# Kernel optimization log

Measured on AMD Instinct MI355X. Metric: run time of the kernel, lower is better.

The kernel has to match this reference:

```python
import jax, jax.numpy as jnp
import numpy as np

B, S, D = 64, 8192, 128  # batch, source length, hidden (enc == dec)


def setup_inputs() -> dict:
    key = jax.random.key(0)
    ks = jax.random.split(key, 7)
    s = 1.0 / np.sqrt(D)
    return {
        "input": jax.random.normal(ks[0], (B, D), jnp.float32),
        "context": jax.random.normal(ks[1], (B, S, D), jnp.float32),
        "W_enc": jax.random.uniform(ks[2], (D, D), jnp.float32, -s, s),
        "b_enc": jax.random.uniform(ks[3], (D,), jnp.float32, -s, s),
        "W_dec": jax.random.uniform(ks[4], (D, D), jnp.float32, -s, s),
        "b_dec": jax.random.uniform(ks[5], (D,), jnp.float32, -s, s),
        "W_out": jax.random.uniform(ks[6], (D, 2 * D), jnp.float32, -s, s),  # no bias
    }


def reference(input, context, W_enc, b_enc, W_dec, b_dec, W_out):
    # projected_context = tanh(lin_encoder(context))  [B, S, D]
    pc = jnp.tanh(jnp.einsum("bse,de->bsd", context, W_enc) + b_enc)
    # q = tanh(lin_decoder(input))  [B, D]
    q = jnp.tanh(input @ W_dec.T + b_dec)
    # attention scores via bmm(projected_context, q): [B, S]
    scores = jnp.einsum("bsd,bd->bs", pc, q)
    attn = jax.nn.softmax(scores, axis=1)  # softmax over source positions
    # weighted sum of (raw) context: [B, D]
    weighted_context = jnp.einsum("bs,bsd->bd", attn, context)
    # h_tilde = tanh(linear_out(concat(weighted_context, q)))  [B, D]
    h_tilde = jnp.tanh(jnp.concatenate([weighted_context, q], axis=-1) @ W_out.T)
    return h_tilde, attn
```

## Files before the change

### kernel.cpp

```cpp
#include <hip/hip_runtime.h>
#include <hip/hip_bf16.h>

#define BB 64
#define SS 8192
#define DD 128

typedef __attribute__((ext_vector_type(8))) short bf16x8;
typedef __attribute__((ext_vector_type(4))) float f32x4;

#define SWZ(c, qd) ((qd) * 16 + ((c) ^ (2 * (qd))))

__device__ __forceinline__ unsigned pk2(float x, float y) {
    __hip_bfloat162 h = __float22bfloat162_rn(make_float2(x, y));
    union { __hip_bfloat162 h2; unsigned u; } cv;
    cv.h2 = h;
    return cv.u;
}

__device__ __forceinline__ float bflo(unsigned p) { return __uint_as_float(p << 16); }
__device__ __forceinline__ float bfhi(unsigned p) { return __uint_as_float(p & 0xffff0000u); }

__device__ __forceinline__ float tanh_fast(float x) {
    float e = __expf(2.f * x);
    return 1.f - 2.f / (e + 1.f);
}

__global__ void qproj_kernel(const float* __restrict__ input,
                             const float* __restrict__ W_dec,
                             const float* __restrict__ b_dec,
                             float* __restrict__ q) {
    __shared__ float xin[DD];
    const int b = blockIdx.x, d = threadIdx.x;
    xin[d] = input[b * DD + d];
    __syncthreads();
    const float4* wrow = (const float4*)(W_dec + (size_t)d * DD);
    float acc = 0.f;
#pragma unroll
    for (int k4 = 0; k4 < DD / 4; k4++) {
        float4 w = wrow[k4];
        float4 x = ((const float4*)xin)[k4];
        acc += w.x * x.x + w.y * x.y + w.z * x.z + w.w * x.w;
    }
    q[b * DD + d] = tanh_fast(acc + b_dec[d]);
}

__global__ __launch_bounds__(256, 3) void score_fused_kernel(
    const float* __restrict__ ctx,
    const float* __restrict__ W_enc,
    const float* __restrict__ b_enc,
    const float* __restrict__ q,
    float* __restrict__ scores,
    float* __restrict__ wcp,
    float* __restrict__ Mp,
    float* __restrict__ Tp) {
    __shared__ __align__(16) short Wl[16384];
    __shared__ __align__(16) short Cl[8192];
    __shared__ float sw[64];
    __shared__ float4 red[256];

    const int t = threadIdx.x;

    const float4* W4 = (const float4*)W_enc;
    for (int c2 = t; c2 < 2048; c2 += 256) {
        int row = c2 >> 4, kc = c2 & 15;
        float4 f0 = W4[row * 32 + kc * 2];
        float4 f1 = W4[row * 32 + kc * 2 + 1];
        int nt = row >> 4, colw = row & 15, kk = kc >> 2, qd = kc & 3;
        int a8 = (nt * 4 + kk) * 128 + SWZ(colw, qd) * 2;
        uint4 u;
        u.x = pk2(f0.x, f0.y); u.y = pk2(f0.z, f0.w);
        u.z = pk2(f1.x, f1.y); u.w = pk2(f1.z, f1.w);
        *(uint4*)&Wl[a8 * 4] = u;
    }

    const int wv = t >> 6, lane = t & 63;
    const int col = lane & 15, quad = lane >> 4;
    const int b = blockIdx.x >> 4;
    const int chunk = blockIdx.x & 15;

    const int u = t & 31, rg = t >> 5;
    const int ukk = u >> 3, uqd = (u >> 1) & 3, uh = u & 1;

    float qv[8], bv[8];
#pragma unroll
    for (int nt = 0; nt < 8; nt++) {
        qv[nt] = q[b * DD + nt * 16 + col];
        bv[nt] = b_enc[nt * 16 + col];
    }

    const float4* base = (const float4*)(ctx + ((size_t)b * SS + (size_t)chunk * 512) * DD);

    float4 R[8];
    auto pack_tile = [&]() {
#pragma unroll
        for (int i = 0; i < 8; i++) {
            int row = rg + 8 * i, w = row >> 4, c = row & 15;
            int a8 = (w * 4 + ukk) * 128 + SWZ(c, uqd) * 2 + uh;
            uint2 pk;
            pk.x = pk2(R[i].x, R[i].y);
            pk.y = pk2(R[i].z, R[i].w);
            *(uint2*)&Cl[a8 * 4] = pk;
        }
    };

#pragma unroll
    for (int i = 0; i < 8; i++) R[i] = base[t + 256 * i];
    pack_tile();
    __syncthreads();

    float Mrun = -INFINITY, Trun = 0.f;
    float4 acc4 = {0.f, 0.f, 0.f, 0.f};

    for (int it = 0; it < 8; ++it) {
        if (it < 7) {
            const float4* tb = base + (size_t)(it + 1) * 2048;
#pragma unroll
            for (int i = 0; i < 8; i++) R[i] = tb[t + 256 * i];
        }

        bf16x8 a[4];
#pragma unroll
        for (int kk = 0; kk < 4; kk++) {
            int a8 = (wv * 4 + kk) * 128 + SWZ(col, quad) * 2;
            a[kk] = *(const bf16x8*)&Cl[a8 * 4];
        }
        f32x4 acc[8];
#pragma unroll
        for (int nt = 0; nt < 8; nt++) {
            f32x4 c = {0.f, 0.f, 0.f, 0.f};
#pragma unroll
            for (int kk = 0; kk < 4; kk++) {
                int a8 = (nt * 4 + kk) * 128 + SWZ(col, quad) * 2;
                bf16x8 bf = *(const bf16x8*)&Wl[a8 * 4];
                c = __builtin_amdgcn_mfma_f32_16x16x32_bf16(a[kk], bf, c, 0, 0, 0);
            }
            acc[nt] = c;
        }

#pragma unroll
        for (int r = 0; r < 4; r++) {
            float v = 0.f;
#pragma unroll
            for (int nt = 0; nt < 8; nt++)
                v += tanh_fast(acc[nt][r] + bv[nt]) * qv[nt];
            v += __shfl_xor(v, 1);
            v += __shfl_xor(v, 2);
            v += __shfl_xor(v, 4);
            v += __shfl_xor(v, 8);
            if (col == 0) {
                int lrow = wv * 16 + quad * 4 + r;
                sw[lrow] = v;
                scores[(size_t)b * SS + chunk * 512 + it * 64 + lrow] = v;
            }
        }
        __syncthreads();

        float sv = sw[lane];
        float m = sv;
#pragma unroll
        for (int off = 1; off < 64; off <<= 1) m = fmaxf(m, __shfl_xor(m, off));
        float Mnew = fmaxf(Mrun, m);
        float alpha = __expf(Mrun - Mnew);
        float wlane = __expf(sv - Mnew);
        float ts = wlane;
#pragma unroll
        for (int off = 1; off < 64; off <<= 1) ts += __shfl_xor(ts, off);
        Trun = Trun * alpha + ts;
        Mrun = Mnew;

        acc4.x *= alpha; acc4.y *= alpha; acc4.z *= alpha; acc4.w *= alpha;
#pragma unroll
        for (int i = 0; i < 8; i++) {
            int row = rg + 8 * i, w = row >> 4, c = row & 15;
            int a8 = (w * 4 + ukk) * 128 + SWZ(c, uqd) * 2 + uh;
            uint2 pk = *(const uint2*)&Cl[a8 * 4];
            float wi = __shfl(wlane, row);
            acc4.x += wi * bflo(pk.x);
            acc4.y += wi * bfhi(pk.x);
            acc4.z += wi * bflo(pk.y);
            acc4.w += wi * bfhi(pk.y);
        }
        __syncthreads();

        if (it < 7) {
            pack_tile();
            __syncthreads();
        }
    }

    red[t] = acc4;
    __syncthreads();
    if (t < 32) {
        float4 s = red[t];
#pragma unroll
        for (int k = 1; k < 8; k++) {
            float4 p = red[t + 32 * k];
            s.x += p.x; s.y += p.y; s.z += p.z; s.w += p.w;
        }
        *(float4*)&wcp[(size_t)blockIdx.x * DD + 4 * t] = s;
    }
    if (t == 0) {
        Mp[blockIdx.x] = Mrun;
        Tp[blockIdx.x] = Trun;
    }
}

__global__ void combine_kernel(const float* __restrict__ wcp,
                               const float* __restrict__ Mp,
                               const float* __restrict__ Tp,
                               float* __restrict__ wc,
                               float* __restrict__ Ms,
                               float* __restrict__ Tinv) {
    const int b = blockIdx.x, d = threadIdx.x;
    float M = -INFINITY;
#pragma unroll
    for (int j = 0; j < 16; j++) M = fmaxf(M, Mp[b * 16 + j]);
    float T = 0.f, acc = 0.f;
#pragma unroll
    for (int j = 0; j < 16; j++) {
        float e = __expf(Mp[b * 16 + j] - M);
        T += Tp[b * 16 + j] * e;
        acc += wcp[(size_t)(b * 16 + j) * DD + d] * e;
    }
    float ti = 1.f / T;
    wc[b * DD + d] = acc * ti;
    if (d == 0) { Ms[b] = M; Tinv[b] = ti; }
}

__global__ __launch_bounds__(512) void attnfin_kernel(const float* __restrict__ scores,
                                                      const float* __restrict__ Ms,
                                                      const float* __restrict__ Tinv,
                                                      float* __restrict__ attn) {
    const int b = blockIdx.x >> 2, seg = blockIdx.x & 3;
    const float M = Ms[b], ti = Tinv[b];
    const float4* s4 = (const float4*)(scores + (size_t)b * SS) + seg * 512;
    float4* a4 = (float4*)(attn + (size_t)b * SS) + seg * 512;
    float4 v = s4[threadIdx.x];
    v.x = __expf(v.x - M) * ti;
    v.y = __expf(v.y - M) * ti;
    v.z = __expf(v.z - M) * ti;
    v.w = __expf(v.w - M) * ti;
    a4[threadIdx.x] = v;
}

__global__ void out_kernel(const float* __restrict__ wc,
                           const float* __restrict__ q,
                           const float* __restrict__ W_out,
                           float* __restrict__ h) {
    __shared__ float cat[2 * DD];
    const int b = blockIdx.x, d = threadIdx.x;
    cat[d] = wc[b * DD + d];
    cat[DD + d] = q[b * DD + d];
    __syncthreads();
    const float4* wrow = (const float4*)(W_out + (size_t)d * 2 * DD);
    float acc = 0.f;
#pragma unroll
    for (int k4 = 0; k4 < 2 * DD / 4; k4++) {
        float4 w = wrow[k4];
        float4 x = ((const float4*)cat)[k4];
        acc += w.x * x.x + w.y * x.y + w.z * x.z + w.w * x.w;
    }
    h[b * DD + d] = tanh_fast(acc);
}

extern "C" void kernel_launch(void* const* d_in, const int* in_sizes, int n_in,
                              void* d_out, int out_size, void* d_ws, size_t ws_size,
                              hipStream_t stream) {
    const float* input = (const float*)d_in[0];
    const float* ctx   = (const float*)d_in[1];
    const float* W_enc = (const float*)d_in[2];
    const float* b_enc = (const float*)d_in[3];
    const float* W_dec = (const float*)d_in[4];
    const float* b_dec = (const float*)d_in[5];
    const float* W_out = (const float*)d_in[6];

    float* h    = (float*)d_out;
    float* attn = (float*)d_out + BB * DD;

    float* ws     = (float*)d_ws;
    float* q      = ws;
    float* wc     = ws + 8192;
    float* scores = ws + 16384;
    float* wcp    = ws + 16384 + 524288;
    float* Mp     = wcp + 1024 * DD;
    float* Tp     = Mp + 1024;
    float* Ms     = Tp + 1024;
    float* Tinv   = Ms + 64;

    qproj_kernel<<<BB, DD, 0, stream>>>(input, W_dec, b_dec, q);
    score_fused_kernel<<<BB * 16, 256, 0, stream>>>(ctx, W_enc, b_enc, q,
                                                    scores, wcp, Mp, Tp);
    combine_kernel<<<BB, DD, 0, stream>>>(wcp, Mp, Tp, wc, Ms, Tinv);
    attnfin_kernel<<<BB * 4, 512, 0, stream>>>(scores, Ms, Tinv, attn);
    out_kernel<<<BB, DD, 0, stream>>>(wc, q, W_out, h);
}
```

Before: 420.9 us.

## Load context directly into MFMA fragments, drop LDS staging, double chunk count

```diff
diff --git a/kernel.cpp b/kernel.cpp
--- a/kernel.cpp
+++ b/kernel.cpp
@@ -4,6 +4,9 @@
 #define BB 64
 #define SS 8192
 #define DD 128
+#define NCHUNK 32
+#define CHROWS 256
+#define NT 4
 
 typedef __attribute__((ext_vector_type(8))) short bf16x8;
 typedef __attribute__((ext_vector_type(4))) float f32x4;
@@ -54,9 +57,8 @@
     float* __restrict__ Mp,
     float* __restrict__ Tp) {
     __shared__ __align__(16) short Wl[16384];
-    __shared__ __align__(16) short Cl[8192];
     __shared__ float sw[64];
-    __shared__ float4 red[256];
+    __shared__ float red[512];
 
     const int t = threadIdx.x;
 
@@ -75,11 +77,8 @@
 
     const int wv = t >> 6, lane = t & 63;
     const int col = lane & 15, quad = lane >> 4;
-    const int b = blockIdx.x >> 4;
-    const int chunk = blockIdx.x & 15;
-
-    const int u = t & 31, rg = t >> 5;
-    const int ukk = u >> 3, uqd = (u >> 1) & 3, uh = u & 1;
+    const int b = blockIdx.x >> 5;
+    const int chunk = blockIdx.x & 31;
 
     float qv[8], bv[8];
 #pragma unroll
@@ -88,61 +87,75 @@
         bv[nt] = b_enc[nt * 16 + col];
     }
 
-    const float4* base = (const float4*)(ctx + ((size_t)b * SS + (size_t)chunk * 512) * DD);
-
-    float4 R[8];
-    auto pack_tile = [&]() {
-#pragma unroll
-        for (int i = 0; i < 8; i++) {
-            int row = rg + 8 * i, w = row >> 4, c = row & 15;
-            int a8 = (w * 4 + ukk) * 128 + SWZ(c, uqd) * 2 + uh;
-            uint2 pk;
-            pk.x = pk2(R[i].x, R[i].y);
-            pk.y = pk2(R[i].z, R[i].w);
-            *(uint2*)&Cl[a8 * 4] = pk;
+    const float4* cbase = (const float4*)ctx
+        + ((size_t)b * SS + (size_t)chunk * CHROWS + wv * 16 + col) * (DD / 4)
+        + quad * 2;
+
+    float4 S[8];
+#pragma unroll
+    for (int kk = 0; kk < 4; kk++) {
+        S[kk * 2]     = cbase[kk * 8];
+        S[kk * 2 + 1] = cbase[kk * 8 + 1];
+    }
+
+    union FU { bf16x8 v; unsigned u[4]; };
+    FU af[4];
+    auto cvt_frags = [&]() {
+#pragma unroll
+        for (int kk = 0; kk < 4; kk++) {
+            float4 f0 = S[kk * 2], f1 = S[kk * 2 + 1];
+            af[kk].u[0] = pk2(f0.x, f0.y);
+            af[kk].u[1] = pk2(f0.z, f0.w);
+            af[kk].u[2] = pk2(f1.x, f1.y);
+            af[kk].u[3] = pk2(f1.z, f1.w);
         }
     };
-
-#pragma unroll
-    for (int i = 0; i < 8; i++) R[i] = base[t + 256 * i];
-    pack_tile();
+    cvt_frags();
     __syncthreads();
 
     float Mrun = -INFINITY, Trun = 0.f;
-    float4 acc4 = {0.f, 0.f, 0.f, 0.f};
-
-    for (int it = 0; it < 8; ++it) {
-        if (it < 7) {
-            const float4* tb = base + (size_t)(it + 1) * 2048;
-#pragma unroll
-            for (int i = 0; i < 8; i++) R[i] = tb[t + 256 * i];
-        }
-
-        bf16x8 a[4];
-#pragma unroll
-        for (int kk = 0; kk < 4; kk++) {
-            int a8 = (wv * 4 + kk) * 128 + SWZ(col, quad) * 2;
-            a[kk] = *(const bf16x8*)&Cl[a8 * 4];
-        }
-        f32x4 acc[8];
-#pragma unroll
-        for (int nt = 0; nt < 8; nt++) {
-            f32x4 c = {0.f, 0.f, 0.f, 0.f};
+    float acc32[32];
+#pragma unroll
+    for (int i = 0; i < 32; i++) acc32[i] = 0.f;
+
+    for (int it = 0; it < NT; ++it) {
+        if (it < NT - 1) {
+            const float4* nb = cbase + (size_t)(it + 1) * (64 * DD / 4);
 #pragma unroll
             for (int kk = 0; kk < 4; kk++) {
-                int a8 = (nt * 4 + kk) * 128 + SWZ(col, quad) * 2;
-                bf16x8 bf = *(const bf16x8*)&Wl[a8 * 4];
-                c = __builtin_amdgcn_mfma_f32_16x16x32_bf16(a[kk], bf, c, 0, 0, 0);
-            }
-            acc[nt] = c;
-        }
-
+                S[kk * 2]     = nb[kk * 8];
+                S[kk * 2 + 1] = nb[kk * 8 + 1];
+            }
+        }
+
+        float vr[4] = {0.f, 0.f, 0.f, 0.f};
+#pragma unroll
+        for (int h = 0; h < 2; h++) {
+            f32x4 acc[4];
+#pragma unroll
+            for (int nt = 0; nt < 4; nt++) {
+                int ntg = h * 4 + nt;
+                f32x4 c = {0.f, 0.f, 0.f, 0.f};
+#pragma unroll
+                for (int kk = 0; kk < 4; kk++) {
+                    int a8 = (ntg * 4 + kk) * 128 + SWZ(col, quad) * 2;
+                    bf16x8 bf = *(const bf16x8*)&Wl[a8 * 4];
+                    c = __builtin_amdgcn_mfma_f32_16x16x32_bf16(af[kk].v, bf, c, 0, 0, 0);
+                }
+                acc[nt] = c;
+            }
+#pragma unroll
+            for (int r = 0; r < 4; r++) {
+#pragma unroll
+                for (int nt = 0; nt < 4; nt++) {
+                    int ntg = h * 4 + nt;
+                    vr[r] += tanh_fast(acc[nt][r] + bv[ntg]) * qv[ntg];
+                }
+            }
+        }
 #pragma unroll
         for (int r = 0; r < 4; r++) {
-            float v = 0.f;
-#pragma unroll
-            for (int nt = 0; nt < 8; nt++)
-                v += tanh_fast(acc[nt][r] + bv[nt]) * qv[nt];
+            float v = vr[r];
             v += __shfl_xor(v, 1);
             v += __shfl_xor(v, 2);
             v += __shfl_xor(v, 4);
@@ -150,7 +163,7 @@
             if (col == 0) {
                 int lrow = wv * 16 + quad * 4 + r;
                 sw[lrow] = v;
-                scores[(size_t)b * SS + chunk * 512 + it * 64 + lrow] = v;
+                scores[(size_t)b * SS + (size_t)chunk * CHROWS + it * 64 + lrow] = v;
             }
         }
         __syncthreads();
@@ -168,36 +181,40 @@
         Trun = Trun * alpha + ts;
         Mrun = Mnew;
 
-        acc4.x *= alpha; acc4.y *= alpha; acc4.z *= alpha; acc4.w *= alpha;
-#pragma unroll
-        for (int i = 0; i < 8; i++) {
-            int row = rg + 8 * i, w = row >> 4, c = row & 15;
-            int a8 = (w * 4 + ukk) * 128 + SWZ(c, uqd) * 2 + uh;
-            uint2 pk = *(const uint2*)&Cl[a8 * 4];
-            float wi = __shfl(wlane, row);
-            acc4.x += wi * bflo(pk.x);
-            acc4.y += wi * bfhi(pk.x);
-            acc4.z += wi * bflo(pk.y);
-            acc4.w += wi * bfhi(pk.y);
-        }
+        float wi = __shfl(wlane, wv * 16 + col);
+#pragma unroll
+        for (int kk = 0; kk < 4; kk++) {
+#pragma unroll
+            for (int w = 0; w < 4; w++) {
+                unsigned pw = af[kk].u[w];
+                acc32[kk * 8 + 2 * w]     = acc32[kk * 8 + 2 * w] * alpha + wi * bflo(pw);
+                acc32[kk * 8 + 2 * w + 1] = acc32[kk * 8 + 2 * w + 1] * alpha + wi * bfhi(pw);
+            }
+        }
+
         __syncthreads();
 
-        if (it < 7) {
-            pack_tile();
-            __syncthreads();
-        }
-    }
-
-    red[t] = acc4;
+        if (it < NT - 1) cvt_frags();
+    }
+
+#pragma unroll
+    for (int i = 0; i < 32; i++) {
+        acc32[i] += __shfl_xor(acc32[i], 1);
+        acc32[i] += __shfl_xor(acc32[i], 2);
+        acc32[i] += __shfl_xor(acc32[i], 4);
+        acc32[i] += __shfl_xor(acc32[i], 8);
+    }
+    if (col == 0) {
+#pragma unroll
+        for (int kk = 0; kk < 4; kk++)
+#pragma unroll
+            for (int j = 0; j < 8; j++)
+                red[wv * 128 + kk * 32 + quad * 8 + j] = acc32[kk * 8 + j];
+    }
     __syncthreads();
-    if (t < 32) {
-        float4 s = red[t];
-#pragma unroll
-        for (int k = 1; k < 8; k++) {
-            float4 p = red[t + 32 * k];
-            s.x += p.x; s.y += p.y; s.z += p.z; s.w += p.w;
-        }
-        *(float4*)&wcp[(size_t)blockIdx.x * DD + 4 * t] = s;
+    if (t < 128) {
+        float s = red[t] + red[128 + t] + red[256 + t] + red[384 + t];
+        wcp[(size_t)blockIdx.x * DD + t] = s;
     }
     if (t == 0) {
         Mp[blockIdx.x] = Mrun;
@@ -205,26 +222,40 @@
     }
 }
 
-__global__ void combine_kernel(const float* __restrict__ wcp,
-                               const float* __restrict__ Mp,
-                               const float* __restrict__ Tp,
-                               float* __restrict__ wc,
-                               float* __restrict__ Ms,
-                               float* __restrict__ Tinv) {
+__global__ void combine_out_kernel(const float* __restrict__ wcp,
+                                   const float* __restrict__ Mp,
+                                   const float* __restrict__ Tp,
+                                   const float* __restrict__ q,
+                                   const float* __restrict__ W_out,
+                                   float* __restrict__ h,
+                                   float* __restrict__ Ms,
+                                   float* __restrict__ Tinv) {
+    __shared__ float cat[2 * DD];
     const int b = blockIdx.x, d = threadIdx.x;
     float M = -INFINITY;
 #pragma unroll
-    for (int j = 0; j < 16; j++) M = fmaxf(M, Mp[b * 16 + j]);
+    for (int j = 0; j < NCHUNK; j++) M = fmaxf(M, Mp[b * NCHUNK + j]);
     float T = 0.f, acc = 0.f;
 #pragma unroll
-    for (int j = 0; j < 16; j++) {
-        float e = __expf(Mp[b * 16 + j] - M);
-        T += Tp[b * 16 + j] * e;
-        acc += wcp[(size_t)(b * 16 + j) * DD + d] * e;
+    for (int j = 0; j < NCHUNK; j++) {
+        float e = __expf(Mp[b * NCHUNK + j] - M);
+        T += Tp[b * NCHUNK + j] * e;
+        acc += wcp[(size_t)(b * NCHUNK + j) * DD + d] * e;
     }
     float ti = 1.f / T;
-    wc[b * DD + d] = acc * ti;
+    cat[d] = acc * ti;
+    cat[DD + d] = q[b * DD + d];
     if (d == 0) { Ms[b] = M; Tinv[b] = ti; }
+    __syncthreads();
+    const float4* wrow = (const float4*)(W_out + (size_t)d * 2 * DD);
+    float a2 = 0.f;
+#pragma unroll
+    for (int k4 = 0; k4 < 2 * DD / 4; k4++) {
+        float4 w = wrow[k4];
+        float4 x = ((const float4*)cat)[k4];
+        a2 += w.x * x.x + w.y * x.y + w.z * x.z + w.w * x.w;
+    }
+    h[b * DD + d] = tanh_fast(a2);
 }
 
 __global__ __launch_bounds__(512) void attnfin_kernel(const float* __restrict__ scores,
@@ -243,26 +274,6 @@
     a4[threadIdx.x] = v;
 }
 
-__global__ void out_kernel(const float* __restrict__ wc,
-                           const float* __restrict__ q,
-                           const float* __restrict__ W_out,
-                           float* __restrict__ h) {
-    __shared__ float cat[2 * DD];
-    const int b = blockIdx.x, d = threadIdx.x;
-    cat[d] = wc[b * DD + d];
-    cat[DD + d] = q[b * DD + d];
-    __syncthreads();
-    const float4* wrow = (const float4*)(W_out + (size_t)d * 2 * DD);
-    float acc = 0.f;
-#pragma unroll
-    for (int k4 = 0; k4 < 2 * DD / 4; k4++) {
-        float4 w = wrow[k4];
-        float4 x = ((const float4*)cat)[k4];
-        acc += w.x * x.x + w.y * x.y + w.z * x.z + w.w * x.w;
-    }
-    h[b * DD + d] = tanh_fast(acc);
-}
-
 extern "C" void kernel_launch(void* const* d_in, const int* in_sizes, int n_in,
                               void* d_out, int out_size, void* d_ws, size_t ws_size,
                               hipStream_t stream) {
@@ -279,18 +290,16 @@
 
     float* ws     = (float*)d_ws;
     float* q      = ws;
-    float* wc     = ws + 8192;
-    float* scores = ws + 16384;
-    float* wcp    = ws + 16384 + 524288;
-    float* Mp     = wcp + 1024 * DD;
-    float* Tp     = Mp + 1024;
-    float* Ms     = Tp + 1024;
+    float* scores = ws + 8192;
+    float* wcp    = scores + 524288;
+    float* Mp     = wcp + 2048 * DD;
+    float* Tp     = Mp + 2048;
+    float* Ms     = Tp + 2048;
     float* Tinv   = Ms + 64;
 
     qproj_kernel<<<BB, DD, 0, stream>>>(input, W_dec, b_dec, q);
-    score_fused_kernel<<<BB * 16, 256, 0, stream>>>(ctx, W_enc, b_enc, q,
-                                                    scores, wcp, Mp, Tp);
-    combine_kernel<<<BB, DD, 0, stream>>>(wcp, Mp, Tp, wc, Ms, Tinv);
+    score_fused_kernel<<<BB * NCHUNK, 256, 0, stream>>>(ctx, W_enc, b_enc, q,
+                                                        scores, wcp, Mp, Tp);
+    combine_out_kernel<<<BB, DD, 0, stream>>>(wcp, Mp, Tp, q, W_out, h, Ms, Tinv);
     attnfin_kernel<<<BB * 4, 512, 0, stream>>>(scores, Ms, Tinv, attn);
-    out_kernel<<<BB, DD, 0, stream>>>(wc, q, W_out, h);
-}
+}
```

Measured after the change: 435.6 us. 1.04x slower.

## Double-buffer context tiles, halve block count, fuse combine with output projection

Applied to the files above, without the earlier changes.

```diff
diff --git a/kernel.cpp b/kernel.cpp
--- a/kernel.cpp
+++ b/kernel.cpp
@@ -4,6 +4,9 @@
 #define BB 64
 #define SS 8192
 #define DD 128
+#define NCHUNK 8
+#define CHROWS 1024
+#define NTILE 16
 
 typedef __attribute__((ext_vector_type(8))) short bf16x8;
 typedef __attribute__((ext_vector_type(4))) float f32x4;
@@ -44,7 +47,7 @@
     q[b * DD + d] = tanh_fast(acc + b_dec[d]);
 }
 
-__global__ __launch_bounds__(256, 3) void score_fused_kernel(
+__global__ __launch_bounds__(256, 2) void score_fused_kernel(
     const float* __restrict__ ctx,
     const float* __restrict__ W_enc,
     const float* __restrict__ b_enc,
@@ -54,7 +57,7 @@
     float* __restrict__ Mp,
     float* __restrict__ Tp) {
     __shared__ __align__(16) short Wl[16384];
-    __shared__ __align__(16) short Cl[8192];
+    __shared__ __align__(16) short Cl[2][8192];
     __shared__ float sw[64];
     __shared__ float4 red[256];
 
@@ -75,8 +78,8 @@
 
     const int wv = t >> 6, lane = t & 63;
     const int col = lane & 15, quad = lane >> 4;
-    const int b = blockIdx.x >> 4;
-    const int chunk = blockIdx.x & 15;
+    const int b = blockIdx.x >> 3;
+    const int chunk = blockIdx.x & 7;
 
     const int u = t & 31, rg = t >> 5;
     const int ukk = u >> 3, uqd = (u >> 1) & 3, uh = u & 1;
@@ -88,10 +91,10 @@
         bv[nt] = b_enc[nt * 16 + col];
     }
 
-    const float4* base = (const float4*)(ctx + ((size_t)b * SS + (size_t)chunk * 512) * DD);
+    const float4* base = (const float4*)(ctx + ((size_t)b * SS + (size_t)chunk * CHROWS) * DD);
 
     float4 R[8];
-    auto pack_tile = [&]() {
+    auto pack_tile = [&](int buf) {
 #pragma unroll
         for (int i = 0; i < 8; i++) {
             int row = rg + 8 * i, w = row >> 4, c = row & 15;
@@ -99,20 +102,21 @@
             uint2 pk;
             pk.x = pk2(R[i].x, R[i].y);
             pk.y = pk2(R[i].z, R[i].w);
-            *(uint2*)&Cl[a8 * 4] = pk;
+            *(uint2*)&Cl[buf][a8 * 4] = pk;
         }
     };
 
 #pragma unroll
     for (int i = 0; i < 8; i++) R[i] = base[t + 256 * i];
-    pack_tile();
+    pack_tile(0);
     __syncthreads();
 
     float Mrun = -INFINITY, Trun = 0.f;
     float4 acc4 = {0.f, 0.f, 0.f, 0.f};
 
-    for (int it = 0; it < 8; ++it) {
-        if (it < 7) {
+    for (int it = 0; it < NTILE; ++it) {
+        const int cur = it & 1;
+        if (it < NTILE - 1) {
             const float4* tb = base + (size_t)(it + 1) * 2048;
 #pragma unroll
             for (int i = 0; i < 8; i++) R[i] = tb[t + 256 * i];
@@ -122,7 +126,7 @@
 #pragma unroll
         for (int kk = 0; kk < 4; kk++) {
             int a8 = (wv * 4 + kk) * 128 + SWZ(col, quad) * 2;
-            a[kk] = *(const bf16x8*)&Cl[a8 * 4];
+            a[kk] = *(const bf16x8*)&Cl[cur][a8 * 4];
         }
         f32x4 acc[8];
 #pragma unroll
@@ -150,7 +154,7 @@
             if (col == 0) {
                 int lrow = wv * 16 + quad * 4 + r;
                 sw[lrow] = v;
-                scores[(size_t)b * SS + chunk * 512 + it * 64 + lrow] = v;
+                scores[(size_t)b * SS + (size_t)chunk * CHROWS + it * 64 + lrow] = v;
             }
         }
         __syncthreads();
@@ -173,19 +177,17 @@
         for (int i = 0; i < 8; i++) {
             int row = rg + 8 * i, w = row >> 4, c = row & 15;
             int a8 = (w * 4 + ukk) * 128 + SWZ(c, uqd) * 2 + uh;
-            uint2 pk = *(const uint2*)&Cl[a8 * 4];
+            uint2 pk = *(const uint2*)&Cl[cur][a8 * 4];
             float wi = __shfl(wlane, row);
             acc4.x += wi * bflo(pk.x);
             acc4.y += wi * bfhi(pk.x);
             acc4.z += wi * bflo(pk.y);
             acc4.w += wi * bfhi(pk.y);
         }
+
+        if (it < NTILE - 1) pack_tile(cur ^ 1);
+
         __syncthreads();
-
-        if (it < 7) {
-            pack_tile();
-            __syncthreads();
-        }
     }
 
     red[t] = acc4;
@@ -205,26 +207,40 @@
     }
 }
 
-__global__ void combine_kernel(const float* __restrict__ wcp,
-                               const float* __restrict__ Mp,
-                               const float* __restrict__ Tp,
-                               float* __restrict__ wc,
-                               float* __restrict__ Ms,
-                               float* __restrict__ Tinv) {
+__global__ void combine_out_kernel(const float* __restrict__ wcp,
+                                   const float* __restrict__ Mp,
+                                   const float* __restrict__ Tp,
+                                   const float* __restrict__ q,
+                                   const float* __restrict__ W_out,
+                                   float* __restrict__ h,
+                                   float* __restrict__ Ms,
+                                   float* __restrict__ Tinv) {
+    __shared__ float cat[2 * DD];
     const int b = blockIdx.x, d = threadIdx.x;
     float M = -INFINITY;
 #pragma unroll
-    for (int j = 0; j < 16; j++) M = fmaxf(M, Mp[b * 16 + j]);
+    for (int j = 0; j < NCHUNK; j++) M = fmaxf(M, Mp[b * NCHUNK + j]);
     float T = 0.f, acc = 0.f;
 #pragma unroll
-    for (int j = 0; j < 16; j++) {
-        float e = __expf(Mp[b * 16 + j] - M);
-        T += Tp[b * 16 + j] * e;
-        acc += wcp[(size_t)(b * 16 + j) * DD + d] * e;
+    for (int j = 0; j < NCHUNK; j++) {
+        float e = __expf(Mp[b * NCHUNK + j] - M);
+        T += Tp[b * NCHUNK + j] * e;
+        acc += wcp[(size_t)(b * NCHUNK + j) * DD + d] * e;
     }
     float ti = 1.f / T;
-    wc[b * DD + d] = acc * ti;
+    cat[d] = acc * ti;
+    cat[DD + d] = q[b * DD + d];
     if (d == 0) { Ms[b] = M; Tinv[b] = ti; }
+    __syncthreads();
+    const float4* wrow = (const float4*)(W_out + (size_t)d * 2 * DD);
+    float a2 = 0.f;
+#pragma unroll
+    for (int k4 = 0; k4 < 2 * DD / 4; k4++) {
+        float4 w = wrow[k4];
+        float4 x = ((const float4*)cat)[k4];
+        a2 += w.x * x.x + w.y * x.y + w.z * x.z + w.w * x.w;
+    }
+    h[b * DD + d] = tanh_fast(a2);
 }
 
 __global__ __launch_bounds__(512) void attnfin_kernel(const float* __restrict__ scores,
@@ -243,26 +259,6 @@
     a4[threadIdx.x] = v;
 }
 
-__global__ void out_kernel(const float* __restrict__ wc,
-                           const float* __restrict__ q,
-                           const float* __restrict__ W_out,
-                           float* __restrict__ h) {
-    __shared__ float cat[2 * DD];
-    const int b = blockIdx.x, d = threadIdx.x;
-    cat[d] = wc[b * DD + d];
-    cat[DD + d] = q[b * DD + d];
-    __syncthreads();
-    const float4* wrow = (const float4*)(W_out + (size_t)d * 2 * DD);
-    float acc = 0.f;
-#pragma unroll
-    for (int k4 = 0; k4 < 2 * DD / 4; k4++) {
-        float4 w = wrow[k4];
-        float4 x = ((const float4*)cat)[k4];
-        acc += w.x * x.x + w.y * x.y + w.z * x.z + w.w * x.w;
-    }
-    h[b * DD + d] = tanh_fast(acc);
-}
-
 extern "C" void kernel_launch(void* const* d_in, const int* in_sizes, int n_in,
                               void* d_out, int out_size, void* d_ws, size_t ws_size,
                               hipStream_t stream) {
@@ -279,18 +275,16 @@
 
     float* ws     = (float*)d_ws;
     float* q      = ws;
-    float* wc     = ws + 8192;
-    float* scores = ws + 16384;
-    float* wcp    = ws + 16384 + 524288;
-    float* Mp     = wcp + 1024 * DD;
-    float* Tp     = Mp + 1024;
-    float* Ms     = Tp + 1024;
+    float* scores = ws + 8192;
+    float* wcp    = scores + 524288;
+    float* Mp     = wcp + 512 * DD;
+    float* Tp     = Mp + 512;
+    float* Ms     = Tp + 512;
     float* Tinv   = Ms + 64;
 
     qproj_kernel<<<BB, DD, 0, stream>>>(input, W_dec, b_dec, q);
-    score_fused_kernel<<<BB * 16, 256, 0, stream>>>(ctx, W_enc, b_enc, q,
-                                                    scores, wcp, Mp, Tp);
-    combine_kernel<<<BB, DD, 0, stream>>>(wcp, Mp, Tp, wc, Ms, Tinv);
+    score_fused_kernel<<<BB * NCHUNK, 256, 0, stream>>>(ctx, W_enc, b_enc, q,
+                                                        scores, wcp, Mp, Tp);
+    combine_out_kernel<<<BB, DD, 0, stream>>>(wcp, Mp, Tp, q, W_out, h, Ms, Tinv);
     attnfin_kernel<<<BB * 4, 512, 0, stream>>>(scores, Ms, Tinv, attn);
-    out_kernel<<<BB, DD, 0, stream>>>(wc, q, W_out, h);
-}
+}
```

After: 400.3 us. 1.05x faster.
